# Kernel tuning notes

Hardware: AMD Instinct MI355X
Metric: run time of the kernel (lower is better)

## Reference

```python
import jax, jax.numpy as jnp
import numpy as np

NH, WS, SS = 8, 7, 3  # num_heads, window_size, shift_size
EPS = 1e-5


def _rel_pos_index(ws):
    coords = np.stack(np.meshgrid(np.arange(ws), np.arange(ws), indexing='ij'))
    coords = coords.reshape(2, -1)                      # [2, L]
    rel = coords[:, :, None] - coords[:, None, :]       # [2, L, L]
    rel = rel.transpose(1, 2, 0) + (ws - 1)
    return rel[..., 0] * (2 * ws - 1) + rel[..., 1]     # [L, L] int


def _attn_mask(H, W, ws, ss):
    # region labels for shifted-window masking (torchvision semantics)
    img = np.zeros((H, W))
    slices = (slice(0, -ws), slice(-ws, -ss), slice(-ss, None))
    cnt = 0
    for hs in slices:
        for wsl in slices:
            img[hs, wsl] = cnt
            cnt += 1
    win = img.reshape(H // ws, ws, W // ws, ws).transpose(0, 2, 1, 3).reshape(-1, ws * ws)
    mask = (win[:, None, :] != win[:, :, None]).astype(np.float32) * (-100.0)
    return mask  # [nWin, L, L]


def _layernorm(x, gamma, beta):
    mu = jnp.mean(x, axis=-1, keepdims=True)
    var = jnp.mean(jnp.square(x - mu), axis=-1, keepdims=True)
    return (x - mu) * jax.lax.rsqrt(var + EPS) * gamma + beta


def _swin_attention(x, qkv_w, qkv_b, proj_w, proj_b, rpb_table):
    B, H, W, C = x.shape
    HD = C // NH
    L = WS * WS
    nH, nW = H // WS, W // WS
    # cyclic shift
    xs = jnp.roll(x, shift=(-SS, -SS), axis=(1, 2))
    # window partition -> [B*nWin, L, C]
    xw = xs.reshape(B, nH, WS, nW, WS, C).transpose(0, 1, 3, 2, 4, 5).reshape(B * nH * nW, L, C)
    qkv = jnp.einsum('nlc,dc->nld', xw, qkv_w) + qkv_b
    qkv = qkv.reshape(-1, L, 3, NH, HD).transpose(2, 0, 3, 1, 4)  # [3, N, h, L, d]
    q, k, v = qkv[0] * (HD ** -0.5), qkv[1], qkv[2]
    attn = jnp.einsum('nhid,nhjd->nhij', q, k)  # [N, h, L, L]
    bias = rpb_table[jnp.asarray(_rel_pos_index(WS))]  # [L, L, h]
    attn = attn + bias.transpose(2, 0, 1)[None]
    mask = jnp.asarray(_attn_mask(H, W, WS, SS))  # [nWin, L, L]
    nwin = nH * nW
    attn = attn.reshape(B, nwin, NH, L, L) + mask[None, :, None]
    attn = jax.nn.softmax(attn.reshape(-1, NH, L, L), axis=-1)
    out = jnp.einsum('nhij,nhjd->nhid', attn, v).transpose(0, 2, 1, 3).reshape(-1, L, C)
    out = jnp.einsum('nlc,dc->nld', out, proj_w) + proj_b
    # reverse windows and shift
    out = out.reshape(B, nH, nW, WS, WS, C).transpose(0, 1, 3, 2, 4, 5).reshape(B, H, W, C)
    return jnp.roll(out, shift=(SS, SS), axis=(1, 2))


def setup_inputs() -> dict:
    key = jax.random.key(0)
    ks = jax.random.split(key, 8)
    B, H, W, C = 32, 56, 56, 256
    F = 4 * C
    s = 0.02
    return {
        'x': jax.random.normal(ks[0], (B, H, W, C), jnp.float32),
        'qkv_w': jax.random.normal(ks[1], (3 * C, C), jnp.float32) * s,
        'qkv_b': jnp.zeros((3 * C,), jnp.float32),
        'proj_w': jax.random.normal(ks[2], (C, C), jnp.float32) * s,
        'proj_b': jnp.zeros((C,), jnp.float32),
        'rpb_table': jax.random.normal(ks[3], ((2 * WS - 1) ** 2, NH), jnp.float32) * s,
        'gamma1': jnp.ones((C,), jnp.float32),
        'beta1': jnp.zeros((C,), jnp.float32),
        'w1': jax.random.normal(ks[4], (C, F), jnp.float32) * s,
        'b1': jax.random.normal(ks[5], (F,), jnp.float32) * 1e-6,
        'w2': jax.random.normal(ks[6], (F, C), jnp.float32) * s,
        'b2': jax.random.normal(ks[7], (C,), jnp.float32) * 1e-6,
        'gamma2': jnp.ones((C,), jnp.float32),
        'beta2': jnp.zeros((C,), jnp.float32),
    }


def reference(x, qkv_w, qkv_b, proj_w, proj_b, rpb_table, gamma1, beta1, w1, b1, w2, b2, gamma2, beta2):
    # post-norm residual block: x + norm1(attn(x)); x + norm2(mlp(x))
    a = _swin_attention(x, qkv_w, qkv_b, proj_w, proj_b, rpb_table)
    x = x + _layernorm(a, gamma1, beta1)
    h = jax.nn.gelu(jnp.einsum('bhwc,cf->bhwf', x, w1) + b1, approximate=False)
    m = jnp.einsum('bhwf,fc->bhwc', h, w2) + b2
    x = x + _layernorm(m, gamma2, beta2)
    return x
```

## Files before the change

### kernel.cpp

```cpp
#include <hip/hip_runtime.h>
#include <hip/hip_bf16.h>


typedef unsigned short ushort_t;
typedef short bf16x8 __attribute__((ext_vector_type(8)));
typedef float f32x4 __attribute__((ext_vector_type(4)));

__device__ __forceinline__ float bf2f(unsigned short u) {
    union { unsigned int i; float f; } x; x.i = ((unsigned int)u) << 16; return x.f;
}
__device__ __forceinline__ unsigned short f2bf(float f) {
    union { float f; unsigned int i; } x; x.f = f;
    unsigned int r = x.i + 0x7fffu + ((x.i >> 16) & 1u);
    return (unsigned short)(r >> 16);
}
__device__ __forceinline__ bf16x8 pack8(float4 a, float4 b) {
    bf16x8 r;
    r[0] = (short)f2bf(a.x); r[1] = (short)f2bf(a.y);
    r[2] = (short)f2bf(a.z); r[3] = (short)f2bf(a.w);
    r[4] = (short)f2bf(b.x); r[5] = (short)f2bf(b.y);
    r[6] = (short)f2bf(b.z); r[7] = (short)f2bf(b.w);
    return r;
}
__device__ __forceinline__ void gl_lds16(const ushort_t* g, ushort_t* l) {
    __builtin_amdgcn_global_load_lds((const __attribute__((address_space(1))) void*)g,
                                     (__attribute__((address_space(3))) void*)l, 16, 0, 0);
}
__device__ __forceinline__ float gelu_f(float v) {
    float s = v * 0.70710678118654752f;
    float ax = fabsf(s);
    float t = __builtin_amdgcn_rcpf(1.0f + 0.3275911f * ax);
    float poly = ((((1.061405429f * t - 1.453152027f) * t + 1.421413741f) * t
                   - 0.284496736f) * t + 0.254829592f) * t;
    float y = 1.0f - poly * __expf(-ax * ax);
    float e = (s < 0.f) ? -y : y;
    return 0.5f * v * (1.0f + e);
}

__device__ __forceinline__ long swin_src_off(int m) {
    int n = m / 49, l = m - n * 49;
    int b = n >> 6, win = n & 63;
    int wh = win >> 3, ww = win & 7;
    int i = l / 7, j = l - i * 7;
    int hs = wh * 7 + i + 3; if (hs >= 56) hs -= 56;
    int ws = ww * 7 + j + 3; if (ws >= 56) ws -= 56;
    return ((long)(b * 56 + hs) * 56 + ws) * 256;
}

template<int SRCT>
__global__ __launch_bounds__(256)
void convW(const float* __restrict__ src, ushort_t* __restrict__ dst, int N, int kshift)
{
    int idx = blockIdx.x * 256 + threadIdx.x;
    int kk = idx & ((1 << kshift) - 1), nn = idx >> kshift;
    float v = SRCT ? src[(long)kk * N + nn] : src[idx];
    dst[idx] = f2bf(v);
}

template<int ACT, int AMODE, int NCOLS>
__global__ __launch_bounds__(256)
void gemm128(const void* __restrict__ Av, const ushort_t* __restrict__ W,
             const float* __restrict__ bias, ushort_t* __restrict__ C,
             int M, int N, int K)
{
    __shared__ ushort_t As[128 * 32];
    __shared__ ushort_t Bs[128 * 32];
    const int t = threadIdx.x, lane = t & 63, wave = t >> 6;
    const int cpx = gridDim.x >> 3;
    const int wg = (blockIdx.x & 7) * cpx + (blockIdx.x >> 3);
    const int row0 = (wg / NCOLS) * 128, col0 = (wg % NCOLS) * 128;
    const int wm = (wave >> 1) * 64, wn = (wave & 1) * 64;

    const ushort_t* ag0; const ushort_t* ag1;
    const float* af0; const float* af1;
    if (AMODE == 0) {
        ag0 = (const ushort_t*)Av + (long)(row0 + (t >> 2)) * K + (t & 3) * 8;
        ag1 = (const ushort_t*)Av + (long)(row0 + 64 + (t >> 2)) * K + (t & 3) * 8;
    } else {
        af0 = (const float*)Av + swin_src_off(row0 + (t >> 2)) + (t & 3) * 8;
        af1 = (const float*)Av + swin_src_off(row0 + 64 + (t >> 2)) + (t & 3) * 8;
    }
    const ushort_t* bg0 = W + (long)(col0 + (t >> 2)) * K + (t & 3) * 8;
    const ushort_t* bg1 = W + (long)(col0 + 64 + (t >> 2)) * K + (t & 3) * 8;
    ushort_t* la0 = &As[t * 8];        ushort_t* la1 = &As[2048 + t * 8];
    ushort_t* lb0 = &Bs[t * 8];        ushort_t* lb1 = &Bs[2048 + t * 8];

    f32x4 acc[4][4] = {};
    for (int k0 = 0; k0 < K; k0 += 32) {
        bf16x8 a0, a1;
        if (AMODE == 1) {
            const float* p0 = af0 + k0;
            const float* p1 = af1 + k0;
            float4 x0 = *(const float4*)p0, x1 = *(const float4*)(p0 + 4);
            float4 x2 = *(const float4*)p1, x3 = *(const float4*)(p1 + 4);
            a0 = pack8(x0, x1); a1 = pack8(x2, x3);
        }
        __syncthreads();
        if (AMODE == 0) {
            gl_lds16(ag0 + k0, la0);
            gl_lds16(ag1 + k0, la1);
        } else {
            *(bf16x8*)la0 = a0;
            *(bf16x8*)la1 = a1;
        }
        gl_lds16(bg0 + k0, lb0);
        gl_lds16(bg1 + k0, lb1);
        __syncthreads();
        bf16x8 af[4], bw[4];
        #pragma unroll
        for (int i = 0; i < 4; i++) {
            af[i] = *(const bf16x8*)&As[(wm + i * 16 + (lane & 15)) * 32 + (lane >> 4) * 8];
            bw[i] = *(const bf16x8*)&Bs[(wn + i * 16 + (lane & 15)) * 32 + (lane >> 4) * 8];
        }
        #pragma unroll
        for (int mi = 0; mi < 4; mi++)
            #pragma unroll
            for (int ni = 0; ni < 4; ni++)
                acc[mi][ni] = __builtin_amdgcn_mfma_f32_16x16x32_bf16(af[mi], bw[ni], acc[mi][ni], 0, 0, 0);
    }
    #pragma unroll
    for (int mi = 0; mi < 4; mi++)
        #pragma unroll
        for (int ni = 0; ni < 4; ni++) {
            const int c = col0 + wn + ni * 16 + (lane & 15);
            const float bv = bias[c];
            #pragma unroll
            for (int r = 0; r < 4; r++) {
                const int rr = row0 + wm + mi * 16 + (lane >> 4) * 4 + r;
                float v = acc[mi][ni][r] + bv;
                if (ACT) v = gelu_f(v);
                C[(long)rr * N + c] = f2bf(v);
            }
        }
}

__global__ __launch_bounds__(64)
void attn_mfma(const ushort_t* __restrict__ qkv, const float* __restrict__ rpb,
               ushort_t* __restrict__ out)
{
    __shared__ ushort_t v_t[32 * 72];
    __shared__ ushort_t p_lds[64 * 72];
    __shared__ float bias_s[169];

    const int blk = blockIdx.x;
    const int n = blk >> 3, h = blk & 7;
    const int l = threadIdx.x;
    const long wbase = (long)n * 49 * 768 + h * 32;
    const float scale = 0.17677669529663687f;

    {
        int j = min(l, 48);
        const ushort_t* vr = qkv + wbase + (long)j * 768 + 512;
        #pragma unroll
        for (int c = 0; c < 4; c++) {
            bf16x8 vv = *(const bf16x8*)(vr + c * 8);
            #pragma unroll
            for (int e = 0; e < 8; e++) v_t[(c * 8 + e) * 72 + l] = (ushort_t)vv[e];
        }
    }
    for (int idx = l; idx < 169; idx += 64) bias_s[idx] = rpb[idx * 8 + h];
    __syncthreads();

    f32x4 s[4][4] = {};
    {
        bf16x8 aq[4], bk[4];
        #pragma unroll
        for (int mt = 0; mt < 4; mt++) {
            int i = min(mt * 16 + (l & 15), 48);
            aq[mt] = *(const bf16x8*)(qkv + wbase + (long)i * 768 + (l >> 4) * 8);
        }
        #pragma unroll
        for (int nt = 0; nt < 4; nt++) {
            int j = min(nt * 16 + (l & 15), 48);
            bk[nt] = *(const bf16x8*)(qkv + wbase + (long)j * 768 + 256 + (l >> 4) * 8);
        }
        #pragma unroll
        for (int mt = 0; mt < 4; mt++)
            #pragma unroll
            for (int nt = 0; nt < 4; nt++)
                s[mt][nt] = __builtin_amdgcn_mfma_f32_16x16x32_bf16(aq[mt], bk[nt], s[mt][nt], 0, 0, 0);
    }

    const int win = n & 63, wh = win >> 3, ww = win & 7;
    int yj[4], xj[4], regj[4]; bool jv[4];
    #pragma unroll
    for (int nt = 0; nt < 4; nt++) {
        int j = nt * 16 + (l & 15);
        jv[nt] = (j <= 48);
        int jc = min(j, 48);
        yj[nt] = jc / 7; xj[nt] = jc - yj[nt] * 7;
        int hs = wh * 7 + yj[nt], wsx = ww * 7 + xj[nt];
        regj[nt] = (hs < 49 ? 0 : (hs < 53 ? 1 : 2)) * 3 + (wsx < 49 ? 0 : (wsx < 53 ? 1 : 2));
    }
    float rinv[4][4];
    #pragma unroll
    for (int mt = 0; mt < 4; mt++) {
        #pragma unroll
        for (int r = 0; r < 4; r++) {
            int i = mt * 16 + (l >> 4) * 4 + r;
            int ic = min(i, 48);
            int yi = ic / 7, xi = ic - yi * 7;
            int hs = wh * 7 + yi, wsx = ww * 7 + xi;
            int regi = (hs < 49 ? 0 : (hs < 53 ? 1 : 2)) * 3 + (wsx < 49 ? 0 : (wsx < 53 ? 1 : 2));
            float val[4];
            #pragma unroll
            for (int nt = 0; nt < 4; nt++) {
                float v = s[mt][nt][r] * scale + bias_s[(yi - yj[nt] + 6) * 13 + (xi - xj[nt] + 6)];
                if (regi != regj[nt]) v -= 100.f;
                val[nt] = jv[nt] ? v : -1e30f;
            }
            float mx = fmaxf(fmaxf(val[0], val[1]), fmaxf(val[2], val[3]));
            #pragma unroll
            for (int off = 1; off <= 8; off <<= 1) mx = fmaxf(mx, __shfl_xor(mx, off));
            float sum = 0.f;
            #pragma unroll
            for (int nt = 0; nt < 4; nt++) { val[nt] = __expf(val[nt] - mx); sum += val[nt]; }
            #pragma unroll
            for (int off = 1; off <= 8; off <<= 1) sum += __shfl_xor(sum, off);
            rinv[mt][r] = 1.0f / sum;
            #pragma unroll
            for (int nt = 0; nt < 4; nt++)
                p_lds[i * 72 + nt * 16 + (l & 15)] = f2bf(val[nt]);
        }
    }
    __syncthreads();

    f32x4 o[4][2] = {};
    #pragma unroll
    for (int ks = 0; ks < 2; ks++) {
        bf16x8 pa[4], vb[2];
        #pragma unroll
        for (int mt = 0; mt < 4; mt++)
            pa[mt] = *(const bf16x8*)&p_lds[(mt * 16 + (l & 15)) * 72 + ks * 32 + (l >> 4) * 8];
        #pragma unroll
        for (int nt = 0; nt < 2; nt++)
            vb[nt] = *(const bf16x8*)&v_t[(nt * 16 + (l & 15)) * 72 + ks * 32 + (l >> 4) * 8];
        #pragma unroll
        for (int mt = 0; mt < 4; mt++)
            #pragma unroll
            for (int nt = 0; nt < 2; nt++)
                o[mt][nt] = __builtin_amdgcn_mfma_f32_16x16x32_bf16(pa[mt], vb[nt], o[mt][nt], 0, 0, 0);
    }
    #pragma unroll
    for (int mt = 0; mt < 4; mt++)
        #pragma unroll
        for (int r = 0; r < 4; r++) {
            int i = mt * 16 + (l >> 4) * 4 + r;
            if (i < 49) {
                float rs = rinv[mt][r];
                #pragma unroll
                for (int nt = 0; nt < 2; nt++) {
                    int d = nt * 16 + (l & 15);
                    out[((long)n * 49 + i) * 256 + h * 32 + d] = f2bf(o[mt][nt][r] * rs);
                }
            }
        }
}

__global__ __launch_bounds__(512)
void projln1(const ushort_t* __restrict__ A, const ushort_t* __restrict__ W,
             const float* __restrict__ pb, const float* __restrict__ x,
             const float* __restrict__ gamma, const float* __restrict__ beta,
             ushort_t* __restrict__ x1b)
{
    __shared__ ushort_t As[128 * 32];
    __shared__ ushort_t Bs[256 * 32];
    __shared__ float red_s[128][4];
    __shared__ float red_ss[128][4];
    __shared__ int srow_s[128];
    const int t = threadIdx.x, lane = t & 63, w = t >> 6;
    const int row0 = blockIdx.x * 128;
    const int wm = (w >> 2) * 64, wn = (w & 3) * 64;

    if (t < 128) srow_s[t] = (int)(swin_src_off(row0 + t) >> 8);

    const ushort_t* ag = A + (long)(row0 + (t >> 2)) * 256 + (t & 3) * 8;
    f32x4 acc[4][4] = {};
    for (int k0 = 0; k0 < 256; k0 += 32) {
        __syncthreads();
        gl_lds16(ag + k0, &As[t * 8]);
        #pragma unroll
        for (int i = 0; i < 2; i++) {
            int u = i * 512 + t;
            gl_lds16(W + (long)(u >> 2) * 256 + k0 + (u & 3) * 8, &Bs[u * 8]);
        }
        __syncthreads();
        bf16x8 af[4], bw[4];
        #pragma unroll
        for (int i2 = 0; i2 < 4; i2++) {
            af[i2] = *(const bf16x8*)&As[(wm + i2 * 16 + (lane & 15)) * 32 + (lane >> 4) * 8];
            bw[i2] = *(const bf16x8*)&Bs[(wn + i2 * 16 + (lane & 15)) * 32 + (lane >> 4) * 8];
        }
        #pragma unroll
        for (int mi = 0; mi < 4; mi++)
            #pragma unroll
            for (int ni = 0; ni < 4; ni++)
                acc[mi][ni] = __builtin_amdgcn_mfma_f32_16x16x32_bf16(af[mi], bw[ni], acc[mi][ni], 0, 0, 0);
    }
    float pbv[4], g1v[4], be1v[4];
    #pragma unroll
    for (int ni = 0; ni < 4; ni++) {
        int col = wn + ni * 16 + (lane & 15);
        pbv[ni] = pb[col]; g1v[ni] = gamma[col]; be1v[ni] = beta[col];
    }
    #pragma unroll
    for (int mi = 0; mi < 4; mi++)
        #pragma unroll
        for (int rr = 0; rr < 4; rr++) {
            float s = 0.f, ss = 0.f;
            #pragma unroll
            for (int ni = 0; ni < 4; ni++) {
                float v = acc[mi][ni][rr] + pbv[ni];
                acc[mi][ni][rr] = v; s += v; ss += v * v;
            }
            #pragma unroll
            for (int off = 1; off <= 8; off <<= 1) { s += __shfl_xor(s, off); ss += __shfl_xor(ss, off); }
            if ((lane & 15) == 0) {
                int r = wm + mi * 16 + (lane >> 4) * 4 + rr;
                red_s[r][w & 3] = s; red_ss[r][w & 3] = ss;
            }
        }
    __syncthreads();
    #pragma unroll
    for (int mi = 0; mi < 4; mi++)
        #pragma unroll
        for (int rr = 0; rr < 4; rr++) {
            const int r = wm + mi * 16 + (lane >> 4) * 4 + rr;
            const float s = red_s[r][0] + red_s[r][1] + red_s[r][2] + red_s[r][3];
            const float ss = red_ss[r][0] + red_ss[r][1] + red_ss[r][2] + red_ss[r][3];
            const float mu = s * (1.0f / 256.0f);
            const float rstd = rsqrtf(ss * (1.0f / 256.0f) - mu * mu + 1e-5f);
            const long sp = srow_s[r];
            #pragma unroll
            for (int ni = 0; ni < 4; ni++) {
                int col = wn + ni * 16 + (lane & 15);
                float o = x[sp * 256 + col] + (acc[mi][ni][rr] - mu) * rstd * g1v[ni] + be1v[ni];
                x1b[sp * 256 + col] = f2bf(o);
            }
        }
}

__global__ __launch_bounds__(256)
void mlp2ln2(const ushort_t* __restrict__ A, const ushort_t* __restrict__ W,
             const float* __restrict__ pb, const ushort_t* __restrict__ x1res,
             const float* __restrict__ gamma, const float* __restrict__ beta,
             float* __restrict__ out)
{
    __shared__ ushort_t As[64 * 32];
    __shared__ ushort_t Bs[256 * 32];
    __shared__ float red_s[64][4];
    __shared__ float red_ss[64][4];
    const int t = threadIdx.x, lane = t & 63, w = t >> 6;
    const int row0 = blockIdx.x * 64;
    const int wn = w * 64;

    const ushort_t* ag = A + (long)(row0 + (t >> 2)) * 1024 + (t & 3) * 8;
    f32x4 acc[4][4] = {};
    for (int k0 = 0; k0 < 1024; k0 += 32) {
        __syncthreads();
        gl_lds16(ag + k0, &As[t * 8]);
        #pragma unroll
        for (int i = 0; i < 4; i++) {
            int u = i * 256 + t;
            gl_lds16(W + (long)(u >> 2) * 1024 + k0 + (u & 3) * 8, &Bs[u * 8]);
        }
        __syncthreads();
        bf16x8 af[4], bw[4];
        #pragma unroll
        for (int i2 = 0; i2 < 4; i2++) {
            af[i2] = *(const bf16x8*)&As[(i2 * 16 + (lane & 15)) * 32 + (lane >> 4) * 8];
            bw[i2] = *(const bf16x8*)&Bs[(wn + i2 * 16 + (lane & 15)) * 32 + (lane >> 4) * 8];
        }
        #pragma unroll
        for (int mi = 0; mi < 4; mi++)
            #pragma unroll
            for (int ni = 0; ni < 4; ni++)
                acc[mi][ni] = __builtin_amdgcn_mfma_f32_16x16x32_bf16(af[mi], bw[ni], acc[mi][ni], 0, 0, 0);
    }
    float pbv[4], g2v[4], be2v[4];
    #pragma unroll
    for (int ni = 0; ni < 4; ni++) {
        int col = wn + ni * 16 + (lane & 15);
        pbv[ni] = pb[col]; g2v[ni] = gamma[col]; be2v[ni] = beta[col];
    }
    #pragma unroll
    for (int mi = 0; mi < 4; mi++)
        #pragma unroll
        for (int rr = 0; rr < 4; rr++) {
            float s = 0.f, ss = 0.f;
            #pragma unroll
            for (int ni = 0; ni < 4; ni++) {
                float v = acc[mi][ni][rr] + pbv[ni];
                acc[mi][ni][rr] = v; s += v; ss += v * v;
            }
            #pragma unroll
            for (int off = 1; off <= 8; off <<= 1) { s += __shfl_xor(s, off); ss += __shfl_xor(ss, off); }
            if ((lane & 15) == 0) {
                int r = mi * 16 + (lane >> 4) * 4 + rr;
                red_s[r][w] = s; red_ss[r][w] = ss;
            }
        }
    __syncthreads();
    #pragma unroll
    for (int mi = 0; mi < 4; mi++)
        #pragma unroll
        for (int rr = 0; rr < 4; rr++) {
            const int r = mi * 16 + (lane >> 4) * 4 + rr;
            const float s = red_s[r][0] + red_s[r][1] + red_s[r][2] + red_s[r][3];
            const float ss = red_ss[r][0] + red_ss[r][1] + red_ss[r][2] + red_ss[r][3];
            const float mu = s * (1.0f / 256.0f);
            const float rstd = rsqrtf(ss * (1.0f / 256.0f) - mu * mu + 1e-5f);
            const long gr = row0 + r;
            #pragma unroll
            for (int ni = 0; ni < 4; ni++) {
                int col = wn + ni * 16 + (lane & 15);
                out[gr * 256 + col] = bf2f(x1res[gr * 256 + col])
                                    + (acc[mi][ni][rr] - mu) * rstd * g2v[ni] + be2v[ni];
            }
        }
}

extern "C" void kernel_launch(void* const* d_in, const int* in_sizes, int n_in,
                              void* d_out, int out_size, void* d_ws, size_t ws_size,
                              hipStream_t stream) {
    const float* x      = (const float*)d_in[0];
    const float* qkv_w  = (const float*)d_in[1];
    const float* qkv_b  = (const float*)d_in[2];
    const float* proj_w = (const float*)d_in[3];
    const float* proj_b = (const float*)d_in[4];
    const float* rpb    = (const float*)d_in[5];
    const float* gamma1 = (const float*)d_in[6];
    const float* beta1  = (const float*)d_in[7];
    const float* w1     = (const float*)d_in[8];
    const float* b1     = (const float*)d_in[9];
    const float* w2     = (const float*)d_in[10];
    const float* b2     = (const float*)d_in[11];
    const float* gamma2 = (const float*)d_in[12];
    const float* beta2  = (const float*)d_in[13];
    float* outf = (float*)d_out;

    ushort_t* attnout = (ushort_t*)d_out;

    char* ws = (char*)d_ws;
    ushort_t* qkvb  = (ushort_t*)ws;
    ushort_t* hbuf  = (ushort_t*)ws;
    ushort_t* x1b   = (ushort_t*)(ws + 154140672ULL);
    ushort_t* wqkvb = (ushort_t*)(ws + 205520896ULL);
    ushort_t* wprojb= (ushort_t*)(ws + 205914112ULL);
    ushort_t* w1t   = (ushort_t*)(ws + 206045184ULL);
    ushort_t* w2t   = (ushort_t*)(ws + 206569472ULL);

    const int M = 100352, MC = 50176;
    dim3 blk(256);
    convW<0><<<dim3(768),  blk, 0, stream>>>(qkv_w,  wqkvb,  768,  8);
    convW<0><<<dim3(256),  blk, 0, stream>>>(proj_w, wprojb, 256,  8);
    convW<1><<<dim3(1024), blk, 0, stream>>>(w1,     w1t,    1024, 8);
    convW<1><<<dim3(1024), blk, 0, stream>>>(w2,     w2t,    256, 10);
    gemm128<0, 1, 6><<<dim3(4704), blk, 0, stream>>>(x, wqkvb, qkv_b, qkvb, M, 768, 256);
    attn_mfma<<<dim3(16384), dim3(64), 0, stream>>>(qkvb, rpb, attnout);
    projln1<<<dim3(784), dim3(512), 0, stream>>>(attnout, wprojb, proj_b, x,
                                                 gamma1, beta1, x1b);
    for (int c2 = 0; c2 < 2; c2++) {
        const long off = (long)c2 * MC * 256;
        gemm128<1, 0, 8><<<dim3(3136), blk, 0, stream>>>(x1b + off, w1t, b1, hbuf, MC, 1024, 256);
        mlp2ln2<<<dim3(784), blk, 0, stream>>>(hbuf, w2t, b2, x1b + off,
                                               gamma2, beta2, outf + off);
    }
}
```

Baseline: 549.8 us.

## Stage full-K tiles in swizzled LDS and overlap halves in the GEMM kernels

The K=256 GEMMs now load the whole K dimension into LDS in two 128-wide halves using an XOR-swizzled layout. The second half is fetched while the first is being multiplied, which replaces the per-32-K double-sync loop. projln1 keeps the full 256x256 projection weight resident in LDS and holds the A fragments in registers. mlp2ln2 switches to 128-wide K steps with swizzled LDS to reduce barriers and bank conflicts. The cost is much higher LDS use per block, which lowers occupancy.

```diff
diff --git a/kernel.cpp b/kernel.cpp
--- a/kernel.cpp
+++ b/kernel.cpp
@@ -5,6 +5,11 @@
 typedef unsigned short ushort_t;
 typedef short bf16x8 __attribute__((ext_vector_type(8)));
 typedef float f32x4 __attribute__((ext_vector_type(4)));
+
+#define WAITV0 asm volatile("s_waitcnt vmcnt(0)" ::: "memory")
+#define WAITL0 asm volatile("s_waitcnt lgkmcnt(0)" ::: "memory")
+#define BAR    __builtin_amdgcn_s_barrier()
+#define SCHED0 __builtin_amdgcn_sched_barrier(0)
 
 __device__ __forceinline__ float bf2f(unsigned short u) {
     union { unsigned int i; float f; } x; x.i = ((unsigned int)u) << 16; return x.f;
@@ -59,65 +64,110 @@
 
 template<int ACT, int AMODE, int NCOLS>
 __global__ __launch_bounds__(256)
-void gemm128(const void* __restrict__ Av, const ushort_t* __restrict__ W,
-             const float* __restrict__ bias, ushort_t* __restrict__ C,
-             int M, int N, int K)
+void gemmFK(const void* __restrict__ Av, const ushort_t* __restrict__ Wg,
+            const float* __restrict__ bias, ushort_t* __restrict__ C, int N)
 {
-    __shared__ ushort_t As[128 * 32];
-    __shared__ ushort_t Bs[128 * 32];
+    __shared__ ushort_t As[2][128][128];
+    __shared__ ushort_t Ws[2][128][128];
     const int t = threadIdx.x, lane = t & 63, wave = t >> 6;
     const int cpx = gridDim.x >> 3;
     const int wg = (blockIdx.x & 7) * cpx + (blockIdx.x >> 3);
     const int row0 = (wg / NCOLS) * 128, col0 = (wg % NCOLS) * 128;
     const int wm = (wave >> 1) * 64, wn = (wave & 1) * 64;
 
-    const ushort_t* ag0; const ushort_t* ag1;
-    const float* af0; const float* af1;
+    f32x4 acc[4][4] = {};
+
+    auto stage_w = [&](int h) {
+        #pragma unroll
+        for (int i = 0; i < 8; i++) {
+            int u = t + i * 256;
+            int rw = u >> 4, b0 = (u & 15) << 4, sw = (rw & 7) << 4;
+            gl_lds16(Wg + (long)(col0 + rw) * 256 + h * 128 + ((b0 ^ sw) >> 1),
+                     (ushort_t*)((char*)Ws + h * 32768 + u * 16));
+        }
+    };
+    auto compute_half = [&](int hh) {
+        #pragma unroll
+        for (int ks2 = 0; ks2 < 4; ks2++) {
+            const int kb = (ks2 * 32 + (lane >> 4) * 8) * 2;
+            bf16x8 af[4], bw[4];
+            #pragma unroll
+            for (int i = 0; i < 4; i++) {
+                const int ra = wm + i * 16 + (lane & 15);
+                af[i] = *(const bf16x8*)((const char*)As + hh * 32768 + ra * 256
+                                         + (kb ^ ((ra & 7) << 4)));
+                const int rb = wn + i * 16 + (lane & 15);
+                bw[i] = *(const bf16x8*)((const char*)Ws + hh * 32768 + rb * 256
+                                         + (kb ^ ((rb & 7) << 4)));
+            }
+            #pragma unroll
+            for (int mi = 0; mi < 4; mi++)
+                #pragma unroll
+                for (int ni = 0; ni < 4; ni++)
+                    acc[mi][ni] = __builtin_amdgcn_mfma_f32_16x16x32_bf16(af[mi], bw[ni], acc[mi][ni], 0, 0, 0);
+        }
+    };
+
     if (AMODE == 0) {
-        ag0 = (const ushort_t*)Av + (long)(row0 + (t >> 2)) * K + (t & 3) * 8;
-        ag1 = (const ushort_t*)Av + (long)(row0 + 64 + (t >> 2)) * K + (t & 3) * 8;
+        const ushort_t* Ag = (const ushort_t*)Av;
+        auto stage_a = [&](int h) {
+            #pragma unroll
+            for (int i = 0; i < 8; i++) {
+                int u = t + i * 256;
+                int rw = u >> 4, b0 = (u & 15) << 4, sw = (rw & 7) << 4;
+                gl_lds16(Ag + (long)(row0 + rw) * 256 + h * 128 + ((b0 ^ sw) >> 1),
+                         (ushort_t*)((char*)As + h * 32768 + u * 16));
+            }
+        };
+        stage_a(0); stage_w(0);
+        WAITV0; BAR; SCHED0;
+        stage_a(1); stage_w(1);
+        compute_half(0);
+        WAITV0; BAR; SCHED0;
+        compute_half(1);
     } else {
-        af0 = (const float*)Av + swin_src_off(row0 + (t >> 2)) + (t & 3) * 8;
-        af1 = (const float*)Av + swin_src_off(row0 + 64 + (t >> 2)) + (t & 3) * 8;
-    }
-    const ushort_t* bg0 = W + (long)(col0 + (t >> 2)) * K + (t & 3) * 8;
-    const ushort_t* bg1 = W + (long)(col0 + 64 + (t >> 2)) * K + (t & 3) * 8;
-    ushort_t* la0 = &As[t * 8];        ushort_t* la1 = &As[2048 + t * 8];
-    ushort_t* lb0 = &Bs[t * 8];        ushort_t* lb1 = &Bs[2048 + t * 8];
-
-    f32x4 acc[4][4] = {};
-    for (int k0 = 0; k0 < K; k0 += 32) {
-        bf16x8 a0, a1;
-        if (AMODE == 1) {
-            const float* p0 = af0 + k0;
-            const float* p1 = af1 + k0;
-            float4 x0 = *(const float4*)p0, x1 = *(const float4*)(p0 + 4);
-            float4 x2 = *(const float4*)p1, x3 = *(const float4*)(p1 + 4);
-            a0 = pack8(x0, x1); a1 = pack8(x2, x3);
-        }
-        __syncthreads();
-        if (AMODE == 0) {
-            gl_lds16(ag0 + k0, la0);
-            gl_lds16(ag1 + k0, la1);
-        } else {
-            *(bf16x8*)la0 = a0;
-            *(bf16x8*)la1 = a1;
-        }
-        gl_lds16(bg0 + k0, lb0);
-        gl_lds16(bg1 + k0, lb1);
-        __syncthreads();
-        bf16x8 af[4], bw[4];
-        #pragma unroll
-        for (int i = 0; i < 4; i++) {
-            af[i] = *(const bf16x8*)&As[(wm + i * 16 + (lane & 15)) * 32 + (lane >> 4) * 8];
-            bw[i] = *(const bf16x8*)&Bs[(wn + i * 16 + (lane & 15)) * 32 + (lane >> 4) * 8];
-        }
-        #pragma unroll
-        for (int mi = 0; mi < 4; mi++)
-            #pragma unroll
-            for (int ni = 0; ni < 4; ni++)
-                acc[mi][ni] = __builtin_amdgcn_mfma_f32_16x16x32_bf16(af[mi], bw[ni], acc[mi][ni], 0, 0, 0);
-    }
+        const int arow = t >> 1, apart = t & 1;
+        const int asw = (arow & 7) << 4;
+        const float* xr = (const float*)Av + swin_src_off(row0 + arow);
+        #pragma unroll
+        for (int j2 = 0; j2 < 8; j2++) {
+            int b = ((apart * 8) + ((j2 + arow) & 7)) << 4;
+            const float* sp = xr + ((b ^ asw) >> 1);
+            *(bf16x8*)((char*)As + arow * 256 + b) =
+                pack8(*(const float4*)sp, *(const float4*)(sp + 4));
+        }
+        stage_w(0);
+        WAITL0; WAITV0; BAR; SCHED0;
+        float4 va0, va1, va2, va3, va4, va5, va6, va7;
+        float4 vb0, vb1, vb2, vb3, vb4, vb5, vb6, vb7;
+        int bj[8];
+        #pragma unroll
+        for (int j2 = 0; j2 < 8; j2++) bj[j2] = ((apart * 8) + ((j2 + arow) & 7)) << 4;
+        {
+            const float* s0 = xr + 128 + ((bj[0] ^ asw) >> 1); va0 = *(const float4*)s0; vb0 = *(const float4*)(s0 + 4);
+            const float* s1 = xr + 128 + ((bj[1] ^ asw) >> 1); va1 = *(const float4*)s1; vb1 = *(const float4*)(s1 + 4);
+            const float* s2 = xr + 128 + ((bj[2] ^ asw) >> 1); va2 = *(const float4*)s2; vb2 = *(const float4*)(s2 + 4);
+            const float* s3 = xr + 128 + ((bj[3] ^ asw) >> 1); va3 = *(const float4*)s3; vb3 = *(const float4*)(s3 + 4);
+            const float* s4 = xr + 128 + ((bj[4] ^ asw) >> 1); va4 = *(const float4*)s4; vb4 = *(const float4*)(s4 + 4);
+            const float* s5 = xr + 128 + ((bj[5] ^ asw) >> 1); va5 = *(const float4*)s5; vb5 = *(const float4*)(s5 + 4);
+            const float* s6 = xr + 128 + ((bj[6] ^ asw) >> 1); va6 = *(const float4*)s6; vb6 = *(const float4*)(s6 + 4);
+            const float* s7 = xr + 128 + ((bj[7] ^ asw) >> 1); va7 = *(const float4*)s7; vb7 = *(const float4*)(s7 + 4);
+        }
+        stage_w(1);
+        compute_half(0);
+        char* a1b = (char*)As + 32768 + arow * 256;
+        *(bf16x8*)(a1b + bj[0]) = pack8(va0, vb0);
+        *(bf16x8*)(a1b + bj[1]) = pack8(va1, vb1);
+        *(bf16x8*)(a1b + bj[2]) = pack8(va2, vb2);
+        *(bf16x8*)(a1b + bj[3]) = pack8(va3, vb3);
+        *(bf16x8*)(a1b + bj[4]) = pack8(va4, vb4);
+        *(bf16x8*)(a1b + bj[5]) = pack8(va5, vb5);
+        *(bf16x8*)(a1b + bj[6]) = pack8(va6, vb6);
+        *(bf16x8*)(a1b + bj[7]) = pack8(va7, vb7);
+        WAITL0; WAITV0; BAR; SCHED0;
+        compute_half(1);
+    }
+
     #pragma unroll
     for (int mi = 0; mi < 4; mi++)
         #pragma unroll
@@ -258,82 +308,91 @@
 }
 
 __global__ __launch_bounds__(512)
-void projln1(const ushort_t* __restrict__ A, const ushort_t* __restrict__ W,
+void projln1(const ushort_t* __restrict__ A, const ushort_t* __restrict__ Wg,
              const float* __restrict__ pb, const float* __restrict__ x,
              const float* __restrict__ gamma, const float* __restrict__ beta,
              ushort_t* __restrict__ x1b)
 {
-    __shared__ ushort_t As[128 * 32];
-    __shared__ ushort_t Bs[256 * 32];
-    __shared__ float red_s[128][4];
-    __shared__ float red_ss[128][4];
+    __shared__ ushort_t Ws[256][256];
+    __shared__ float red_s[128][2];
+    __shared__ float red_ss[128][2];
     __shared__ int srow_s[128];
     const int t = threadIdx.x, lane = t & 63, w = t >> 6;
+    const int rowg = w >> 1, colg = w & 1;
     const int row0 = blockIdx.x * 128;
-    const int wm = (w >> 2) * 64, wn = (w & 3) * 64;
 
     if (t < 128) srow_s[t] = (int)(swin_src_off(row0 + t) >> 8);
 
-    const ushort_t* ag = A + (long)(row0 + (t >> 2)) * 256 + (t & 3) * 8;
-    f32x4 acc[4][4] = {};
-    for (int k0 = 0; k0 < 256; k0 += 32) {
-        __syncthreads();
-        gl_lds16(ag + k0, &As[t * 8]);
-        #pragma unroll
-        for (int i = 0; i < 2; i++) {
-            int u = i * 512 + t;
-            gl_lds16(W + (long)(u >> 2) * 256 + k0 + (u & 3) * 8, &Bs[u * 8]);
-        }
-        __syncthreads();
-        bf16x8 af[4], bw[4];
-        #pragma unroll
-        for (int i2 = 0; i2 < 4; i2++) {
-            af[i2] = *(const bf16x8*)&As[(wm + i2 * 16 + (lane & 15)) * 32 + (lane >> 4) * 8];
-            bw[i2] = *(const bf16x8*)&Bs[(wn + i2 * 16 + (lane & 15)) * 32 + (lane >> 4) * 8];
-        }
-        #pragma unroll
-        for (int mi = 0; mi < 4; mi++)
-            #pragma unroll
-            for (int ni = 0; ni < 4; ni++)
-                acc[mi][ni] = __builtin_amdgcn_mfma_f32_16x16x32_bf16(af[mi], bw[ni], acc[mi][ni], 0, 0, 0);
-    }
-    float pbv[4], g1v[4], be1v[4];
-    #pragma unroll
-    for (int ni = 0; ni < 4; ni++) {
-        int col = wn + ni * 16 + (lane & 15);
+    #pragma unroll
+    for (int i = 0; i < 16; i++) {
+        int u = t + i * 512;
+        int nr = u >> 5, b0 = (u & 31) << 4, sw = (nr & 7) << 4;
+        gl_lds16(Wg + (long)nr * 256 + ((b0 ^ sw) >> 1),
+                 (ushort_t*)((char*)Ws + u * 16));
+    }
+    bf16x8 xa[2][8];
+    #pragma unroll
+    for (int mi = 0; mi < 2; mi++)
+        #pragma unroll
+        for (int ks = 0; ks < 8; ks++)
+            xa[mi][ks] = *(const bf16x8*)(A + (long)(row0 + rowg * 32 + mi * 16 + (lane & 15)) * 256
+                                          + ks * 32 + (lane >> 4) * 8);
+    WAITL0; WAITV0; BAR; SCHED0;
+
+    f32x4 acc[2][8] = {};
+    #pragma unroll
+    for (int ks = 0; ks < 8; ks++) {
+        const int kb = (ks * 32 + (lane >> 4) * 8) * 2;
+        bf16x8 bw[8];
+        #pragma unroll
+        for (int ni = 0; ni < 8; ni++) {
+            const int nr = colg * 128 + ni * 16 + (lane & 15);
+            bw[ni] = *(const bf16x8*)((const char*)Ws + nr * 512 + (kb ^ ((nr & 7) << 4)));
+        }
+        #pragma unroll
+        for (int mi = 0; mi < 2; mi++)
+            #pragma unroll
+            for (int ni = 0; ni < 8; ni++)
+                acc[mi][ni] = __builtin_amdgcn_mfma_f32_16x16x32_bf16(xa[mi][ks], bw[ni], acc[mi][ni], 0, 0, 0);
+    }
+
+    float pbv[8], g1v[8], be1v[8];
+    #pragma unroll
+    for (int ni = 0; ni < 8; ni++) {
+        int col = colg * 128 + ni * 16 + (lane & 15);
         pbv[ni] = pb[col]; g1v[ni] = gamma[col]; be1v[ni] = beta[col];
     }
     #pragma unroll
-    for (int mi = 0; mi < 4; mi++)
+    for (int mi = 0; mi < 2; mi++)
         #pragma unroll
         for (int rr = 0; rr < 4; rr++) {
             float s = 0.f, ss = 0.f;
             #pragma unroll
-            for (int ni = 0; ni < 4; ni++) {
+            for (int ni = 0; ni < 8; ni++) {
                 float v = acc[mi][ni][rr] + pbv[ni];
                 acc[mi][ni][rr] = v; s += v; ss += v * v;
             }
             #pragma unroll
             for (int off = 1; off <= 8; off <<= 1) { s += __shfl_xor(s, off); ss += __shfl_xor(ss, off); }
             if ((lane & 15) == 0) {
-                int r = wm + mi * 16 + (lane >> 4) * 4 + rr;
-                red_s[r][w & 3] = s; red_ss[r][w & 3] = ss;
+                int r = rowg * 32 + mi * 16 + (lane >> 4) * 4 + rr;
+                red_s[r][colg] = s; red_ss[r][colg] = ss;
             }
         }
     __syncthreads();
     #pragma unroll
-    for (int mi = 0; mi < 4; mi++)
+    for (int mi = 0; mi < 2; mi++)
         #pragma unroll
         for (int rr = 0; rr < 4; rr++) {
-            const int r = wm + mi * 16 + (lane >> 4) * 4 + rr;
-            const float s = red_s[r][0] + red_s[r][1] + red_s[r][2] + red_s[r][3];
-            const float ss = red_ss[r][0] + red_ss[r][1] + red_ss[r][2] + red_ss[r][3];
+            const int r = rowg * 32 + mi * 16 + (lane >> 4) * 4 + rr;
+            const float s = red_s[r][0] + red_s[r][1];
+            const float ss = red_ss[r][0] + red_ss[r][1];
             const float mu = s * (1.0f / 256.0f);
             const float rstd = rsqrtf(ss * (1.0f / 256.0f) - mu * mu + 1e-5f);
             const long sp = srow_s[r];
             #pragma unroll
-            for (int ni = 0; ni < 4; ni++) {
-                int col = wn + ni * 16 + (lane & 15);
+            for (int ni = 0; ni < 8; ni++) {
+                int col = colg * 128 + ni * 16 + (lane & 15);
                 float o = x[sp * 256 + col] + (acc[mi][ni][rr] - mu) * rstd * g1v[ni] + be1v[ni];
                 x1b[sp * 256 + col] = f2bf(o);
             }
@@ -341,41 +400,54 @@
 }
 
 __global__ __launch_bounds__(256)
-void mlp2ln2(const ushort_t* __restrict__ A, const ushort_t* __restrict__ W,
+void mlp2ln2(const ushort_t* __restrict__ A, const ushort_t* __restrict__ Wg,
              const float* __restrict__ pb, const ushort_t* __restrict__ x1res,
              const float* __restrict__ gamma, const float* __restrict__ beta,
              float* __restrict__ out)
 {
-    __shared__ ushort_t As[64 * 32];
-    __shared__ ushort_t Bs[256 * 32];
+    __shared__ ushort_t As[64][128];
+    __shared__ ushort_t Ws[256][128];
     __shared__ float red_s[64][4];
     __shared__ float red_ss[64][4];
     const int t = threadIdx.x, lane = t & 63, w = t >> 6;
     const int row0 = blockIdx.x * 64;
     const int wn = w * 64;
 
-    const ushort_t* ag = A + (long)(row0 + (t >> 2)) * 1024 + (t & 3) * 8;
     f32x4 acc[4][4] = {};
-    for (int k0 = 0; k0 < 1024; k0 += 32) {
+    for (int k0 = 0; k0 < 1024; k0 += 128) {
         __syncthreads();
-        gl_lds16(ag + k0, &As[t * 8]);
         #pragma unroll
         for (int i = 0; i < 4; i++) {
-            int u = i * 256 + t;
-            gl_lds16(W + (long)(u >> 2) * 1024 + k0 + (u & 3) * 8, &Bs[u * 8]);
+            int u = t + i * 256;
+            int rw = u >> 4, b0 = (u & 15) << 4, sw = (rw & 7) << 4;
+            gl_lds16(A + (long)(row0 + rw) * 1024 + k0 + ((b0 ^ sw) >> 1),
+                     (ushort_t*)((char*)As + u * 16));
+        }
+        #pragma unroll
+        for (int i = 0; i < 16; i++) {
+            int u = t + i * 256;
+            int nr = u >> 4, b0 = (u & 15) << 4, sw = (nr & 7) << 4;
+            gl_lds16(Wg + (long)nr * 1024 + k0 + ((b0 ^ sw) >> 1),
+                     (ushort_t*)((char*)Ws + u * 16));
         }
         __syncthreads();
-        bf16x8 af[4], bw[4];
-        #pragma unroll
-        for (int i2 = 0; i2 < 4; i2++) {
-            af[i2] = *(const bf16x8*)&As[(i2 * 16 + (lane & 15)) * 32 + (lane >> 4) * 8];
-            bw[i2] = *(const bf16x8*)&Bs[(wn + i2 * 16 + (lane & 15)) * 32 + (lane >> 4) * 8];
-        }
-        #pragma unroll
-        for (int mi = 0; mi < 4; mi++)
-            #pragma unroll
-            for (int ni = 0; ni < 4; ni++)
-                acc[mi][ni] = __builtin_amdgcn_mfma_f32_16x16x32_bf16(af[mi], bw[ni], acc[mi][ni], 0, 0, 0);
+        #pragma unroll
+        for (int kss = 0; kss < 4; kss++) {
+            const int kb = (kss * 32 + (lane >> 4) * 8) * 2;
+            bf16x8 af[4], bw[4];
+            #pragma unroll
+            for (int i2 = 0; i2 < 4; i2++) {
+                const int ra = i2 * 16 + (lane & 15);
+                af[i2] = *(const bf16x8*)((const char*)As + ra * 256 + (kb ^ ((ra & 7) << 4)));
+                const int rb = wn + i2 * 16 + (lane & 15);
+                bw[i2] = *(const bf16x8*)((const char*)Ws + rb * 256 + (kb ^ ((rb & 7) << 4)));
+            }
+            #pragma unroll
+            for (int mi = 0; mi < 4; mi++)
+                #pragma unroll
+                for (int ni = 0; ni < 4; ni++)
+                    acc[mi][ni] = __builtin_amdgcn_mfma_f32_16x16x32_bf16(af[mi], bw[ni], acc[mi][ni], 0, 0, 0);
+        }
     }
     float pbv[4], g2v[4], be2v[4];
     #pragma unroll
@@ -450,19 +522,19 @@
     ushort_t* w1t   = (ushort_t*)(ws + 206045184ULL);
     ushort_t* w2t   = (ushort_t*)(ws + 206569472ULL);
 
-    const int M = 100352, MC = 50176;
+    const int MC = 50176;
     dim3 blk(256);
     convW<0><<<dim3(768),  blk, 0, stream>>>(qkv_w,  wqkvb,  768,  8);
     convW<0><<<dim3(256),  blk, 0, stream>>>(proj_w, wprojb, 256,  8);
     convW<1><<<dim3(1024), blk, 0, stream>>>(w1,     w1t,    1024, 8);
     convW<1><<<dim3(1024), blk, 0, stream>>>(w2,     w2t,    256, 10);
-    gemm128<0, 1, 6><<<dim3(4704), blk, 0, stream>>>(x, wqkvb, qkv_b, qkvb, M, 768, 256);
+    gemmFK<0, 1, 6><<<dim3(4704), blk, 0, stream>>>(x, wqkvb, qkv_b, qkvb, 768);
     attn_mfma<<<dim3(16384), dim3(64), 0, stream>>>(qkvb, rpb, attnout);
     projln1<<<dim3(784), dim3(512), 0, stream>>>(attnout, wprojb, proj_b, x,
                                                  gamma1, beta1, x1b);
     for (int c2 = 0; c2 < 2; c2++) {
         const long off = (long)c2 * MC * 256;
-        gemm128<1, 0, 8><<<dim3(3136), blk, 0, stream>>>(x1b + off, w1t, b1, hbuf, MC, 1024, 256);
+        gemmFK<1, 0, 8><<<dim3(3136), blk, 0, stream>>>(x1b + off, w1t, b1, hbuf, 1024);
         mlp2ln2<<<dim3(784), blk, 0, stream>>>(hbuf, w2t, b2, x1b + off,
                                                gamma2, beta2, outf + off);
     }
```

After: 728.7 us. 32.6% more time.

## Double-buffer LDS tiles with XOR swizzle and pre-gather shifted input to bf16

Applied to the files above, without the earlier changes.

All three GEMM-style kernels move to double-buffered LDS: the next K-tile is prefetched with direct global-to-LDS loads while MFMAs run on the current tile, leaving one barrier per iteration instead of two. LDS rows get an XOR swizzle on the 16-byte chunk index to reduce bank conflicts on the fragment reads. A new xgather kernel performs the cyclic-shift/window gather and fp32-to-bf16 conversion once into a scratch area of the output buffer, so the QKV GEMM reads contiguous bf16 through the async-load path. This doubles LDS use, which may lower occupancy, and adds an extra pass over the input.

```diff
diff --git a/kernel.cpp b/kernel.cpp
--- a/kernel.cpp
+++ b/kernel.cpp
@@ -5,6 +5,9 @@
 typedef unsigned short ushort_t;
 typedef short bf16x8 __attribute__((ext_vector_type(8)));
 typedef float f32x4 __attribute__((ext_vector_type(4)));
+
+#define WAITV0 asm volatile("s_waitcnt vmcnt(0)" ::: "memory")
+#define BAR    __builtin_amdgcn_s_barrier()
 
 __device__ __forceinline__ float bf2f(unsigned short u) {
     union { unsigned int i; float f; } x; x.i = ((unsigned int)u) << 16; return x.f;
@@ -47,6 +50,15 @@
     return ((long)(b * 56 + hs) * 56 + ws) * 256;
 }
 
+__global__ __launch_bounds__(256)
+void xgather(const float* __restrict__ x, ushort_t* __restrict__ xg)
+{
+    int t = blockIdx.x * 256 + threadIdx.x;
+    int row = t >> 5, ch = (t & 31) * 8;
+    const float* src = x + swin_src_off(row) + ch;
+    *(bf16x8*)(xg + (long)row * 256 + ch) = pack8(*(const float4*)src, *(const float4*)(src + 4));
+}
+
 template<int SRCT>
 __global__ __launch_bounds__(256)
 void convW(const float* __restrict__ src, ushort_t* __restrict__ dst, int N, int kshift)
@@ -57,60 +69,66 @@
     dst[idx] = f2bf(v);
 }
 
-template<int ACT, int AMODE, int NCOLS>
+template<int ACT, int NCOLS>
 __global__ __launch_bounds__(256)
-void gemm128(const void* __restrict__ Av, const ushort_t* __restrict__ W,
+void gemm128(const ushort_t* __restrict__ A, const ushort_t* __restrict__ W,
              const float* __restrict__ bias, ushort_t* __restrict__ C,
              int M, int N, int K)
 {
-    __shared__ ushort_t As[128 * 32];
-    __shared__ ushort_t Bs[128 * 32];
+    __shared__ ushort_t As[2][128 * 32];
+    __shared__ ushort_t Bs[2][128 * 32];
     const int t = threadIdx.x, lane = t & 63, wave = t >> 6;
     const int cpx = gridDim.x >> 3;
     const int wg = (blockIdx.x & 7) * cpx + (blockIdx.x >> 3);
     const int row0 = (wg / NCOLS) * 128, col0 = (wg % NCOLS) * 128;
     const int wm = (wave >> 1) * 64, wn = (wave & 1) * 64;
 
-    const ushort_t* ag0; const ushort_t* ag1;
-    const float* af0; const float* af1;
-    if (AMODE == 0) {
-        ag0 = (const ushort_t*)Av + (long)(row0 + (t >> 2)) * K + (t & 3) * 8;
-        ag1 = (const ushort_t*)Av + (long)(row0 + 64 + (t >> 2)) * K + (t & 3) * 8;
-    } else {
-        af0 = (const float*)Av + swin_src_off(row0 + (t >> 2)) + (t & 3) * 8;
-        af1 = (const float*)Av + swin_src_off(row0 + 64 + (t >> 2)) + (t & 3) * 8;
-    }
-    const ushort_t* bg0 = W + (long)(col0 + (t >> 2)) * K + (t & 3) * 8;
-    const ushort_t* bg1 = W + (long)(col0 + 64 + (t >> 2)) * K + (t & 3) * 8;
-    ushort_t* la0 = &As[t * 8];        ushort_t* la1 = &As[2048 + t * 8];
-    ushort_t* lb0 = &Bs[t * 8];        ushort_t* lb1 = &Bs[2048 + t * 8];
+    const int u0 = t, u1 = t + 256;
+    const int r0 = u0 >> 2, s0 = ((u0 & 3) ^ ((r0 >> 1) & 3)) * 8;
+    const int r1 = u1 >> 2, s1 = ((u1 & 3) ^ ((r1 >> 1) & 3)) * 8;
+    const ushort_t* a0 = A + (long)(row0 + r0) * K + s0;
+    const ushort_t* a1 = A + (long)(row0 + r1) * K + s1;
+    const ushort_t* b0 = W + (long)(col0 + r0) * K + s0;
+    const ushort_t* b1 = W + (long)(col0 + r1) * K + s1;
+
+    int offA[4], offB[4];
+    #pragma unroll
+    for (int i = 0; i < 4; i++) {
+        int ra = wm + i * 16 + (lane & 15);
+        offA[i] = ra * 32 + (((lane >> 4) ^ ((ra >> 1) & 3)) * 8);
+        int rb = wn + i * 16 + (lane & 15);
+        offB[i] = rb * 32 + (((lane >> 4) ^ ((rb >> 1) & 3)) * 8);
+    }
 
     f32x4 acc[4][4] = {};
-    for (int k0 = 0; k0 < K; k0 += 32) {
-        bf16x8 a0, a1;
-        if (AMODE == 1) {
-            const float* p0 = af0 + k0;
-            const float* p1 = af1 + k0;
-            float4 x0 = *(const float4*)p0, x1 = *(const float4*)(p0 + 4);
-            float4 x2 = *(const float4*)p1, x3 = *(const float4*)(p1 + 4);
-            a0 = pack8(x0, x1); a1 = pack8(x2, x3);
-        }
-        __syncthreads();
-        if (AMODE == 0) {
-            gl_lds16(ag0 + k0, la0);
-            gl_lds16(ag1 + k0, la1);
-        } else {
-            *(bf16x8*)la0 = a0;
-            *(bf16x8*)la1 = a1;
-        }
-        gl_lds16(bg0 + k0, lb0);
-        gl_lds16(bg1 + k0, lb1);
-        __syncthreads();
+    gl_lds16(a0, &As[0][u0 * 8]); gl_lds16(a1, &As[0][u1 * 8]);
+    gl_lds16(b0, &Bs[0][u0 * 8]); gl_lds16(b1, &Bs[0][u1 * 8]);
+    WAITV0; BAR;
+    const int nk = K >> 5;
+    for (int kt = 0; kt < nk - 1; kt++) {
+        const int cur = kt & 1, nxt = cur ^ 1, k1 = (kt + 1) * 32;
+        gl_lds16(a0 + k1, &As[nxt][u0 * 8]); gl_lds16(a1 + k1, &As[nxt][u1 * 8]);
+        gl_lds16(b0 + k1, &Bs[nxt][u0 * 8]); gl_lds16(b1 + k1, &Bs[nxt][u1 * 8]);
         bf16x8 af[4], bw[4];
         #pragma unroll
         for (int i = 0; i < 4; i++) {
-            af[i] = *(const bf16x8*)&As[(wm + i * 16 + (lane & 15)) * 32 + (lane >> 4) * 8];
-            bw[i] = *(const bf16x8*)&Bs[(wn + i * 16 + (lane & 15)) * 32 + (lane >> 4) * 8];
+            af[i] = *(const bf16x8*)&As[cur][offA[i]];
+            bw[i] = *(const bf16x8*)&Bs[cur][offB[i]];
+        }
+        #pragma unroll
+        for (int mi = 0; mi < 4; mi++)
+            #pragma unroll
+            for (int ni = 0; ni < 4; ni++)
+                acc[mi][ni] = __builtin_amdgcn_mfma_f32_16x16x32_bf16(af[mi], bw[ni], acc[mi][ni], 0, 0, 0);
+        WAITV0; BAR;
+    }
+    {
+        const int cur = (nk - 1) & 1;
+        bf16x8 af[4], bw[4];
+        #pragma unroll
+        for (int i = 0; i < 4; i++) {
+            af[i] = *(const bf16x8*)&As[cur][offA[i]];
+            bw[i] = *(const bf16x8*)&Bs[cur][offB[i]];
         }
         #pragma unroll
         for (int mi = 0; mi < 4; mi++)
@@ -263,8 +281,8 @@
              const float* __restrict__ gamma, const float* __restrict__ beta,
              ushort_t* __restrict__ x1b)
 {
-    __shared__ ushort_t As[128 * 32];
-    __shared__ ushort_t Bs[256 * 32];
+    __shared__ ushort_t As[2][128 * 32];
+    __shared__ ushort_t Bs[2][256 * 32];
     __shared__ float red_s[128][4];
     __shared__ float red_ss[128][4];
     __shared__ int srow_s[128];
@@ -274,29 +292,58 @@
 
     if (t < 128) srow_s[t] = (int)(swin_src_off(row0 + t) >> 8);
 
-    const ushort_t* ag = A + (long)(row0 + (t >> 2)) * 256 + (t & 3) * 8;
+    const int ra0 = t >> 2, sa0 = ((t & 3) ^ ((ra0 >> 1) & 3)) * 8;
+    const ushort_t* ag = A + (long)(row0 + ra0) * 256 + sa0;
+    const int ub0 = t, ub1 = t + 512;
+    const int rb0 = ub0 >> 2, sb0 = ((ub0 & 3) ^ ((rb0 >> 1) & 3)) * 8;
+    const int rb1 = ub1 >> 2, sb1 = ((ub1 & 3) ^ ((rb1 >> 1) & 3)) * 8;
+    const ushort_t* bg0 = W + (long)rb0 * 256 + sb0;
+    const ushort_t* bg1 = W + (long)rb1 * 256 + sb1;
+
+    int offA[4], offB[4];
+    #pragma unroll
+    for (int i = 0; i < 4; i++) {
+        int ra = wm + i * 16 + (lane & 15);
+        offA[i] = ra * 32 + (((lane >> 4) ^ ((ra >> 1) & 3)) * 8);
+        int rb = wn + i * 16 + (lane & 15);
+        offB[i] = rb * 32 + (((lane >> 4) ^ ((rb >> 1) & 3)) * 8);
+    }
+
     f32x4 acc[4][4] = {};
-    for (int k0 = 0; k0 < 256; k0 += 32) {
-        __syncthreads();
-        gl_lds16(ag + k0, &As[t * 8]);
-        #pragma unroll
-        for (int i = 0; i < 2; i++) {
-            int u = i * 512 + t;
-            gl_lds16(W + (long)(u >> 2) * 256 + k0 + (u & 3) * 8, &Bs[u * 8]);
-        }
-        __syncthreads();
+    gl_lds16(ag, &As[0][t * 8]);
+    gl_lds16(bg0, &Bs[0][ub0 * 8]); gl_lds16(bg1, &Bs[0][ub1 * 8]);
+    WAITV0; BAR;
+    for (int kt = 0; kt < 7; kt++) {
+        const int cur = kt & 1, nxt = cur ^ 1, k1 = (kt + 1) * 32;
+        gl_lds16(ag + k1, &As[nxt][t * 8]);
+        gl_lds16(bg0 + k1, &Bs[nxt][ub0 * 8]); gl_lds16(bg1 + k1, &Bs[nxt][ub1 * 8]);
         bf16x8 af[4], bw[4];
         #pragma unroll
-        for (int i2 = 0; i2 < 4; i2++) {
-            af[i2] = *(const bf16x8*)&As[(wm + i2 * 16 + (lane & 15)) * 32 + (lane >> 4) * 8];
-            bw[i2] = *(const bf16x8*)&Bs[(wn + i2 * 16 + (lane & 15)) * 32 + (lane >> 4) * 8];
+        for (int i = 0; i < 4; i++) {
+            af[i] = *(const bf16x8*)&As[cur][offA[i]];
+            bw[i] = *(const bf16x8*)&Bs[cur][offB[i]];
         }
         #pragma unroll
         for (int mi = 0; mi < 4; mi++)
             #pragma unroll
             for (int ni = 0; ni < 4; ni++)
                 acc[mi][ni] = __builtin_amdgcn_mfma_f32_16x16x32_bf16(af[mi], bw[ni], acc[mi][ni], 0, 0, 0);
-    }
+        WAITV0; BAR;
+    }
+    {
+        bf16x8 af[4], bw[4];
+        #pragma unroll
+        for (int i = 0; i < 4; i++) {
+            af[i] = *(const bf16x8*)&As[1][offA[i]];
+            bw[i] = *(const bf16x8*)&Bs[1][offB[i]];
+        }
+        #pragma unroll
+        for (int mi = 0; mi < 4; mi++)
+            #pragma unroll
+            for (int ni = 0; ni < 4; ni++)
+                acc[mi][ni] = __builtin_amdgcn_mfma_f32_16x16x32_bf16(af[mi], bw[ni], acc[mi][ni], 0, 0, 0);
+    }
+
     float pbv[4], g1v[4], be1v[4];
     #pragma unroll
     for (int ni = 0; ni < 4; ni++) {
@@ -346,30 +393,63 @@
              const float* __restrict__ gamma, const float* __restrict__ beta,
              float* __restrict__ out)
 {
-    __shared__ ushort_t As[64 * 32];
-    __shared__ ushort_t Bs[256 * 32];
+    __shared__ ushort_t As[2][64 * 32];
+    __shared__ ushort_t Bs[2][256 * 32];
     __shared__ float red_s[64][4];
     __shared__ float red_ss[64][4];
     const int t = threadIdx.x, lane = t & 63, w = t >> 6;
     const int row0 = blockIdx.x * 64;
     const int wn = w * 64;
 
-    const ushort_t* ag = A + (long)(row0 + (t >> 2)) * 1024 + (t & 3) * 8;
+    const int ra0 = t >> 2, sa0 = ((t & 3) ^ ((ra0 >> 1) & 3)) * 8;
+    const ushort_t* ag = A + (long)(row0 + ra0) * 1024 + sa0;
+    const ushort_t* bg[4];
+    int ub[4];
+    #pragma unroll
+    for (int i = 0; i < 4; i++) {
+        ub[i] = t + i * 256;
+        int rb = ub[i] >> 2, sb = ((ub[i] & 3) ^ ((rb >> 1) & 3)) * 8;
+        bg[i] = W + (long)rb * 1024 + sb;
+    }
+
+    int offA[4], offB[4];
+    #pragma unroll
+    for (int i = 0; i < 4; i++) {
+        int ra = i * 16 + (lane & 15);
+        offA[i] = ra * 32 + (((lane >> 4) ^ ((ra >> 1) & 3)) * 8);
+        int rb = wn + i * 16 + (lane & 15);
+        offB[i] = rb * 32 + (((lane >> 4) ^ ((rb >> 1) & 3)) * 8);
+    }
+
     f32x4 acc[4][4] = {};
-    for (int k0 = 0; k0 < 1024; k0 += 32) {
-        __syncthreads();
-        gl_lds16(ag + k0, &As[t * 8]);
-        #pragma unroll
-        for (int i = 0; i < 4; i++) {
-            int u = i * 256 + t;
-            gl_lds16(W + (long)(u >> 2) * 1024 + k0 + (u & 3) * 8, &Bs[u * 8]);
-        }
-        __syncthreads();
+    gl_lds16(ag, &As[0][t * 8]);
+    #pragma unroll
+    for (int i = 0; i < 4; i++) gl_lds16(bg[i], &Bs[0][ub[i] * 8]);
+    WAITV0; BAR;
+    for (int kt = 0; kt < 31; kt++) {
+        const int cur = kt & 1, nxt = cur ^ 1, k1 = (kt + 1) * 32;
+        gl_lds16(ag + k1, &As[nxt][t * 8]);
+        #pragma unroll
+        for (int i = 0; i < 4; i++) gl_lds16(bg[i] + k1, &Bs[nxt][ub[i] * 8]);
         bf16x8 af[4], bw[4];
         #pragma unroll
         for (int i2 = 0; i2 < 4; i2++) {
-            af[i2] = *(const bf16x8*)&As[(i2 * 16 + (lane & 15)) * 32 + (lane >> 4) * 8];
-            bw[i2] = *(const bf16x8*)&Bs[(wn + i2 * 16 + (lane & 15)) * 32 + (lane >> 4) * 8];
+            af[i2] = *(const bf16x8*)&As[cur][offA[i2]];
+            bw[i2] = *(const bf16x8*)&Bs[cur][offB[i2]];
+        }
+        #pragma unroll
+        for (int mi = 0; mi < 4; mi++)
+            #pragma unroll
+            for (int ni = 0; ni < 4; ni++)
+                acc[mi][ni] = __builtin_amdgcn_mfma_f32_16x16x32_bf16(af[mi], bw[ni], acc[mi][ni], 0, 0, 0);
+        WAITV0; BAR;
+    }
+    {
+        bf16x8 af[4], bw[4];
+        #pragma unroll
+        for (int i2 = 0; i2 < 4; i2++) {
+            af[i2] = *(const bf16x8*)&As[1][offA[i2]];
+            bw[i2] = *(const bf16x8*)&Bs[1][offB[i2]];
         }
         #pragma unroll
         for (int mi = 0; mi < 4; mi++)
@@ -439,7 +519,9 @@
     const float* beta2  = (const float*)d_in[13];
     float* outf = (float*)d_out;
 
-    ushort_t* attnout = (ushort_t*)d_out;
+    char* ob = (char*)d_out;
+    ushort_t* xg      = (ushort_t*)ob;
+    ushort_t* attnout = (ushort_t*)(ob + 51380224ULL);
 
     char* ws = (char*)d_ws;
     ushort_t* qkvb  = (ushort_t*)ws;
@@ -452,17 +534,18 @@
 
     const int M = 100352, MC = 50176;
     dim3 blk(256);
+    xgather<<<dim3(M / 8), blk, 0, stream>>>(x, xg);
     convW<0><<<dim3(768),  blk, 0, stream>>>(qkv_w,  wqkvb,  768,  8);
     convW<0><<<dim3(256),  blk, 0, stream>>>(proj_w, wprojb, 256,  8);
     convW<1><<<dim3(1024), blk, 0, stream>>>(w1,     w1t,    1024, 8);
     convW<1><<<dim3(1024), blk, 0, stream>>>(w2,     w2t,    256, 10);
-    gemm128<0, 1, 6><<<dim3(4704), blk, 0, stream>>>(x, wqkvb, qkv_b, qkvb, M, 768, 256);
+    gemm128<0, 6><<<dim3(4704), blk, 0, stream>>>(xg, wqkvb, qkv_b, qkvb, M, 768, 256);
     attn_mfma<<<dim3(16384), dim3(64), 0, stream>>>(qkvb, rpb, attnout);
     projln1<<<dim3(784), dim3(512), 0, stream>>>(attnout, wprojb, proj_b, x,
                                                  gamma1, beta1, x1b);
     for (int c2 = 0; c2 < 2; c2++) {
         const long off = (long)c2 * MC * 256;
-        gemm128<1, 0, 8><<<dim3(3136), blk, 0, stream>>>(x1b + off, w1t, b1, hbuf, MC, 1024, 256);
+        gemm128<1, 8><<<dim3(3136), blk, 0, stream>>>(x1b + off, w1t, b1, hbuf, MC, 1024, 256);
         mlp2ln2<<<dim3(784), blk, 0, stream>>>(hbuf, w2t, b2, x1b + off,
                                                gamma2, beta2, outf + off);
     }
```

Measured after the change: 547.0 us. About the same (-0.5%).
